# Optimization experiments

Measured on AMD Instinct MI355X. Metric: run time of the kernel, lower is better.

The kernel has to match this reference:

```python
import jax, jax.numpy as jnp
import numpy as np

B, S, NH, D_IN = 64, 512, 4, 256   # batch, seq_len, rnn n_head, input_dim
H = 256                            # hidden_dim == attention activation_dim
AH = 256                           # attention_hidden_dim (attn out_dim)
OUT = 3                            # output_dim (sentiment classes)


def setup_inputs() -> dict:
    key = jax.random.key(0)
    ks = jax.random.split(key, 9)
    def p(k, shape, scale=0.05):
        return jax.random.normal(k, shape, dtype=jnp.float32) * scale
    return dict(
        x=jax.random.normal(ks[0], (B, S, NH, D_IN), dtype=jnp.float32),
        Wk=p(ks[1], (D_IN, H)), bk=jnp.zeros((H,), jnp.float32),
        Wq=p(ks[2], (H, H)),    bq=jnp.zeros((H,), jnp.float32),
        w_mlp=p(ks[3], (2 * H,)),
        Wproj=p(ks[4], (H, AH)), bproj=jnp.zeros((AH,), jnp.float32),
        W1=p(ks[5], (D_IN + AH, H)), b1=jnp.zeros((H,), jnp.float32),
        W2=p(ks[6], (H, H)),    b2=jnp.zeros((H,), jnp.float32),
        Wo=p(ks[7], (NH * H, OUT)), bo=jnp.zeros((OUT,), jnp.float32),
    )


def _cell(x_t, hidden, params):
    Wk, bk, Wq, bq, w_mlp, Wproj, bproj, W1, b1, W2, b2, Wo, bo = params
    kx = x_t @ Wk + bk           # [B, NH, H]  keys from step input
    qx = hidden @ Wq + bq        # [B, NH, H]  queries from hidden state
    w1, w2 = w_mlp[:H], w_mlp[H:]
    # MLP score: s[b,i,j] = tanh(cat(kx[b,j], qx[b,i]) . w) = tanh(kx[b,j].w1 + qx[b,i].w2)
    score = jnp.tanh((qx @ w2)[:, :, None] + (kx @ w1)[:, None, :])  # [B, NH, NH]
    score = jax.nn.softmax(score, axis=-1)
    attn = jnp.einsum('bij,bjh->bih', score, kx) @ Wproj + bproj     # [B, NH, AH]
    concat = jnp.concatenate([x_t, attn], axis=-1)                   # [B, NH, D_IN+AH]
    hidden_new = jax.nn.relu(concat @ W1 + b1) @ W2 + b2             # [B, NH, H]
    logits = hidden_new.reshape(B, NH * H) @ Wo + bo                 # [B, OUT]
    out = jax.nn.log_softmax(logits, axis=-1)
    return out, hidden_new


def reference(x, Wk, bk, Wq, bq, w_mlp, Wproj, bproj, W1, b1, W2, b2, Wo, bo):
    params = (Wk, bk, Wq, bq, w_mlp, Wproj, bproj, W1, b1, W2, b2, Wo, bo)
    h0 = jnp.zeros((B, NH, H), x.dtype)
    xs = jnp.swapaxes(x, 0, 1)  # [S, B, NH, D_IN] for scan over time
    def step(h, x_t):
        out, h_new = _cell(x_t, h, params)
        return h_new, out
    h_final, outs = jax.lax.scan(step, h0, xs)
    # return_sequence=False: last-step log-softmax output and final hidden
    return outs[-1], h_final
```

## Files before the change

### kernel.cpp

```cpp
#include <hip/hip_runtime.h>
#include <hip/hip_bf16.h>
#include <math.h>

#define BB   64
#define SS   512
#define NHH  4
#define DD   256
#define HH   256
#define LDH  264

typedef __attribute__((ext_vector_type(8))) short  short8;
typedef __attribute__((ext_vector_type(4))) float  floatx4;

#define OFF_V2     0
#define OFF_CB1    256
#define OFF_C2     512
#define OFF_CKW    513
#define OFF_QW     768
#define OFF_WK1    1024
#define OFF_BKP    1280
#define OFF_VT     1536
#define OFF_RU     1792
#define OFF_WFUSE  67328
#define OFF_WKF    132864
#define OFF_PACK   198400
#define OFF_CH     263936

__device__ __forceinline__ unsigned short f2b(float f) {
  __hip_bfloat16 h = __float2bfloat16(f);
  return __builtin_bit_cast(unsigned short, h);
}
__device__ __forceinline__ float b2f(unsigned short u) {
  unsigned v = (unsigned)u << 16;
  return __builtin_bit_cast(float, v);
}

__global__ __launch_bounds__(256) void initA_kernel(
    const float* __restrict__ Wproj, const float* __restrict__ W1,
    const float* __restrict__ bk, const float* __restrict__ bproj,
    const float* __restrict__ Wq, const float* __restrict__ w_mlp,
    float* __restrict__ ws)
{
  int tid = threadIdx.x;
  int bx = blockIdx.x;
  const float* W1b = W1 + 256 * 256;
  if (bx < 256) {
    __shared__ float row[256];
    row[tid] = Wproj[bx * 256 + tid];
    __syncthreads();
    float acc = 0.f;
#pragma unroll 8
    for (int k = 0; k < 256; ++k)
      acc = fmaf(row[k], W1b[k * 256 + tid], acc);
    ws[OFF_WFUSE + bx * 256 + tid] = acc;
  } else if (bx == 256) {
    float acc = bproj[tid];
#pragma unroll 8
    for (int k = 0; k < 256; ++k)
      acc = fmaf(bk[k], Wproj[k * 256 + tid], acc);
    ws[OFF_BKP + tid] = acc;
  } else {
    const float4* Wq4 = (const float4*)(Wq + tid * 256);
    const float4* w24 = (const float4*)(w_mlp + 256);
    float a = 0.f;
    for (int k = 0; k < 64; ++k) {
      float4 wv = Wq4[k], xv = w24[k];
      a = fmaf(wv.x, xv.x, fmaf(wv.y, xv.y, fmaf(wv.z, xv.z, fmaf(wv.w, xv.w, a))));
    }
    ws[OFF_VT + tid] = a;
  }
}

__global__ __launch_bounds__(256) void initB_kernel(
    const float* __restrict__ Wk, const float* __restrict__ W1,
    const float* __restrict__ b1, const float* __restrict__ W2,
    const float* __restrict__ b2, const float* __restrict__ bq,
    const float* __restrict__ bk, const float* __restrict__ w_mlp,
    float* __restrict__ ws)
{
  int tid = threadIdx.x;
  int bx = blockIdx.x;
  if (bx < 256) {
    __shared__ float row[256];
    row[tid] = Wk[bx * 256 + tid];
    __syncthreads();
    float acc = 0.f;
    const float* Wf = ws + OFF_WFUSE;
#pragma unroll 8
    for (int k = 0; k < 256; ++k)
      acc = fmaf(row[k], Wf[k * 256 + tid], acc);
    ws[OFF_WKF + bx * 256 + tid] = acc;
  } else if (bx == 256) {
    const float* W1b = W1 + 256 * 256;
    float acc = b1[tid];
#pragma unroll 8
    for (int k = 0; k < 256; ++k)
      acc = fmaf(ws[OFF_BKP + k], W1b[k * 256 + tid], acc);
    ws[OFF_CB1 + tid] = acc;
  } else if (bx == 257) {
    __shared__ float red[256];
    {
      const float4* W24 = (const float4*)(W2 + tid * 256);
      const float4* v4  = (const float4*)(ws + OFF_VT);
      float a = 0.f;
      for (int k = 0; k < 64; ++k) {
        float4 wv = W24[k], xv = v4[k];
        a = fmaf(wv.x, xv.x, fmaf(wv.y, xv.y, fmaf(wv.z, xv.z, fmaf(wv.w, xv.w, a))));
      }
      ws[OFF_V2 + tid] = a;
    }
    red[tid] = bq[tid] * w_mlp[256 + tid];
    __syncthreads();
    for (int s = 128; s; s >>= 1) { if (tid < s) red[tid] += red[tid + s]; __syncthreads(); }
    float s2 = red[0];
    __syncthreads();
    ws[OFF_QW + tid] = s2;
    red[tid] = b2[tid] * ws[OFF_VT + tid];
    __syncthreads();
    for (int s = 128; s; s >>= 1) { if (tid < s) red[tid] += red[tid + s]; __syncthreads(); }
    if (tid == 0) ws[OFF_C2] = red[0] + s2;
    __syncthreads();
    red[tid] = bk[tid] * w_mlp[tid];
    __syncthreads();
    for (int s = 128; s; s >>= 1) { if (tid < s) red[tid] += red[tid + s]; __syncthreads(); }
    if (tid == 0) ws[OFF_CKW] = red[0];
  } else {
    const float4* Wk4 = (const float4*)(Wk + tid * 256);
    const float4* w14 = (const float4*)(w_mlp);
    float a = 0.f;
    for (int k = 0; k < 64; ++k) {
      float4 wv = Wk4[k], xv = w14[k];
      a = fmaf(wv.x, xv.x, fmaf(wv.y, xv.y, fmaf(wv.z, xv.z, fmaf(wv.w, xv.w, a))));
    }
    ws[OFF_WK1 + tid] = a;
  }
}

__global__ __launch_bounds__(256) void initC_kernel(
    const float* __restrict__ W1, float* __restrict__ ws)
{
  int idx = blockIdx.x * 256 + threadIdx.x;
  int mat = idx >> 16;
  int rem = idx & 65535;
  int j    = rem & 7;
  int lane = (rem >> 3) & 63;
  int ks   = (rem >> 9) & 7;
  int pan  = rem >> 12;
  int k = ks * 32 + ((lane >> 4) << 3) + j;
  int n = pan * 16 + (lane & 15);
  float v = (mat == 0) ? ws[OFF_WKF + k * 256 + n] : W1[k * 256 + n];
  ((unsigned short*)(ws + OFF_PACK))[idx] = f2b(v);
}

__device__ __forceinline__ void mfma_gemm4(
    const unsigned short* A_lds, const short8* __restrict__ Bp,
    const float* __restrict__ bias, floatx4 acc[4][4], int l, int w)
{
  int col = l & 15, quad = l >> 4;
#pragma unroll
  for (int pp = 0; pp < 4; ++pp) {
    float bv = bias ? bias[(w * 4 + pp) * 16 + col] : 0.f;
#pragma unroll
    for (int mf = 0; mf < 4; ++mf)
      acc[mf][pp] = (floatx4){bv, bv, bv, bv};
  }
  const short8* Bb = Bp + (size_t)(w * 4) * 512 + l;
  short8 bb[3][4];
#pragma unroll
  for (int pp = 0; pp < 4; ++pp) bb[0][pp] = Bb[pp * 512];
#pragma unroll
  for (int pp = 0; pp < 4; ++pp) bb[1][pp] = Bb[pp * 512 + 64];
#pragma unroll
  for (int kb = 0; kb < 8; ++kb) {
    if (kb + 2 < 8) {
#pragma unroll
      for (int pp = 0; pp < 4; ++pp)
        bb[(kb + 2) % 3][pp] = Bb[pp * 512 + (kb + 2) * 64];
    }
    short8 aa[4];
#pragma unroll
    for (int mf = 0; mf < 4; ++mf)
      aa[mf] = *(const short8*)(A_lds + (mf * 16 + col) * LDH + kb * 32 + quad * 8);
#pragma unroll
    for (int mf = 0; mf < 4; ++mf)
#pragma unroll
      for (int pp = 0; pp < 4; ++pp)
        acc[mf][pp] = __builtin_amdgcn_mfma_f32_16x16x32_bf16(
            aa[mf], bb[kb % 3][pp], acc[mf][pp], 0, 0, 0);
  }
}

__device__ __forceinline__ void acc_to_lds(
    unsigned short* D, const floatx4 acc[4][4], int l, int w)
{
  int col = l & 15, quad = l >> 4;
#pragma unroll
  for (int mf = 0; mf < 4; ++mf)
#pragma unroll
    for (int pp = 0; pp < 4; ++pp)
#pragma unroll
      for (int r = 0; r < 4; ++r)
        D[(mf * 16 + quad * 4 + r) * LDH + (w * 4 + pp) * 16 + col] = f2b(acc[mf][pp][r]);
}

__device__ __forceinline__ void lds_to_global_bf16(
    const unsigned short* S, unsigned short* __restrict__ g, int b, int tt, int tid)
{
#pragma unroll
  for (int it = 0; it < 8; ++it) {
    int u8 = it * 256 + tid;
    int r = u8 >> 5;
    int c8 = u8 & 31;
    int t = tt * 16 + (r >> 2), head = r & 3;
    float4 v = *(const float4*)&S[r * LDH + c8 * 8];
    *(float4*)&g[(((size_t)t * 64 + b) * 4 + head) * 256 + c8 * 8] = v;
  }
}

__global__ __launch_bounds__(256, 2) void pre_kernel(
    const float* __restrict__ x, const float* __restrict__ ws,
    float* __restrict__ kw_c, unsigned short* __restrict__ xw1_c,
    unsigned short* __restrict__ kpw_c, int t0)
{
  __shared__ float kwbuf[256];
  __shared__ __align__(16) unsigned short XS[64 * LDH];

  int b  = blockIdx.x & 63;
  int tt = blockIdx.x >> 6;
  int tid = threadIdx.x;
  int l = tid & 63, w = tid >> 6;

  const float4* xsrc = (const float4*)(x + (size_t)(b * SS + t0 + tt * 16) * NHH * DD);
#pragma unroll
  for (int i = 0; i < 16; ++i) {
    int f4 = i * 256 + tid;
    int r = f4 >> 6, c4 = f4 & 63;
    float4 v = xsrc[f4];
    ushort4 h;
    h.x = f2b(v.x); h.y = f2b(v.y); h.z = f2b(v.z); h.w = f2b(v.w);
    *(ushort4*)&XS[r * LDH + c4 * 4] = h;
  }
  __syncthreads();

  const short8* wp0 = (const short8*)((const unsigned short*)(ws + OFF_PACK));
  const short8* wp1 = (const short8*)((const unsigned short*)(ws + OFF_PACK) + 65536);

  {
    float part = 0.f;
    const unsigned short* trow = XS + l * LDH + w * 64;
#pragma unroll
    for (int j8 = 0; j8 < 8; ++j8) {
      short8 tv = *(const short8*)(trow + j8 * 8);
#pragma unroll
      for (int j = 0; j < 8; ++j)
        part = fmaf(b2f((unsigned short)tv[j]), ws[OFF_WK1 + w * 64 + j8 * 8 + j], part);
    }
    kwbuf[l * 4 + w] = part;
  }

  floatx4 acc1[4][4], acc2[4][4];
  mfma_gemm4(XS, wp0, nullptr, acc1, l, w);
  mfma_gemm4(XS, wp1, ws + OFF_CB1, acc2, l, w);
  __syncthreads();

  if (tid < 64) {
    float s = kwbuf[tid * 4] + kwbuf[tid * 4 + 1] + kwbuf[tid * 4 + 2] + kwbuf[tid * 4 + 3]
            + ws[OFF_CKW];
    kw_c[((size_t)(tt * 16 + (tid >> 2)) * 64 + b) * 4 + (tid & 3)] = s;
  }

  acc_to_lds(XS, acc1, l, w);
  __syncthreads();
  lds_to_global_bf16(XS, kpw_c, b, tt, tid);
  __syncthreads();
  acc_to_lds(XS, acc2, l, w);
  __syncthreads();
  lds_to_global_bf16(XS, xw1_c, b, tt, tid);
}

__device__ __forceinline__ float wave_reduce_sum(float x) {
#define DPPSTEP(ctrl, rmask)                                                   \
  {                                                                            \
    int _s = __builtin_amdgcn_update_dpp(0, __builtin_bit_cast(int, x),        \
                                         (ctrl), (rmask), 0xf, true);          \
    x += __builtin_bit_cast(float, _s);                                        \
  }
  DPPSTEP(0x111, 0xf)
  DPPSTEP(0x112, 0xf)
  DPPSTEP(0x114, 0xf)
  DPPSTEP(0x118, 0xf)
  DPPSTEP(0x142, 0xa)
  DPPSTEP(0x143, 0xc)
#undef DPPSTEP
  return __builtin_bit_cast(float, __builtin_amdgcn_readlane(__builtin_bit_cast(int, x), 63));
}

__device__ __forceinline__ float tanh_fast(float y) {
  float ex = __expf(2.f * y);
  return 1.f - 2.f * __builtin_amdgcn_rcpf(ex + 1.f);
}

__global__ __launch_bounds__(256, 1) void seq_kernel(
    const unsigned short* __restrict__ xw1_c, const unsigned short* __restrict__ kpw_c,
    const float* __restrict__ kw_c, float* __restrict__ ws,
    float* __restrict__ relu_u, int t0, int n)
{
  int b = blockIdx.x & 63;
  int i = blockIdx.x >> 6;
  int tid = threadIdx.x;
  int wv = tid >> 6, l = tid & 63;
  int ngroups = n >> 3;

  if (wv == 0) {
    float4 v2v = ((const float4*)(ws + OFF_V2))[l];
    float c2 = ws[OFF_C2];
    float qw = ws[OFF_QW + b * 4 + i];

    const ushort4* xw = (const ushort4*)xw1_c;
    const ushort4* kp = (const ushort4*)kpw_c;

    struct Slot { ushort4 x, k0, k1, k2, k3; float4 kw; };

    auto load = [&](Slot& s, int tc) {
      size_t rb_ = (size_t)(tc * 64 + b) * 4;
      s.x  = xw[(rb_ + i) * 64 + l];
      s.k0 = kp[(rb_ + 0) * 64 + l];
      s.k1 = kp[(rb_ + 1) * 64 + l];
      s.k2 = kp[(rb_ + 2) * 64 + l];
      s.k3 = kp[(rb_ + 3) * 64 + l];
      s.kw = *(const float4*)&kw_c[rb_];
    };

    auto step = [&](Slot& s, int t) {
      float e0 = tanh_fast(qw + s.kw.x);
      float e1 = tanh_fast(qw + s.kw.y);
      float e2 = tanh_fast(qw + s.kw.z);
      float e3 = tanh_fast(qw + s.kw.w);
      float q0 = __expf(e0), q1 = __expf(e1), q2 = __expf(e2), q3 = __expf(e3);
      float inv = __builtin_amdgcn_rcpf(q0 + q1 + q2 + q3);
      float4 K0 = {b2f(s.k0.x), b2f(s.k0.y), b2f(s.k0.z), b2f(s.k0.w)};
      float4 K1 = {b2f(s.k1.x), b2f(s.k1.y), b2f(s.k1.z), b2f(s.k1.w)};
      float4 K2 = {b2f(s.k2.x), b2f(s.k2.y), b2f(s.k2.z), b2f(s.k2.w)};
      float4 K3 = {b2f(s.k3.x), b2f(s.k3.y), b2f(s.k3.z), b2f(s.k3.w)};
      float4 X  = {b2f(s.x.x), b2f(s.x.y), b2f(s.x.z), b2f(s.x.w)};
      float4 a;
      a.x = fmaf(q0, K0.x, fmaf(q1, K1.x, fmaf(q2, K2.x, q3 * K3.x)));
      a.y = fmaf(q0, K0.y, fmaf(q1, K1.y, fmaf(q2, K2.y, q3 * K3.y)));
      a.z = fmaf(q0, K0.z, fmaf(q1, K1.z, fmaf(q2, K2.z, q3 * K3.z)));
      a.w = fmaf(q0, K0.w, fmaf(q1, K1.w, fmaf(q2, K2.w, q3 * K3.w)));
      float4 u;
      u.x = fmaf(a.x, inv, X.x); u.y = fmaf(a.y, inv, X.y);
      u.z = fmaf(a.z, inv, X.z); u.w = fmaf(a.w, inv, X.w);
      float4 r;
      r.x = fmaxf(u.x, 0.f); r.y = fmaxf(u.y, 0.f);
      r.z = fmaxf(u.z, 0.f); r.w = fmaxf(u.w, 0.f);
      float d = fmaf(r.x, v2v.x, fmaf(r.y, v2v.y, fmaf(r.z, v2v.z, r.w * v2v.w)));
      qw = wave_reduce_sum(d) + c2;
      if (t0 + t == SS - 1)
        *(float4*)&relu_u[(size_t)(b * 4 + i) * 256 + l * 4] = r;
    };

    Slot s[8];
#pragma unroll
    for (int j = 0; j < 8; ++j) load(s[j], j < n ? j : n - 1);

    for (int g = 0; g < ngroups; ++g) {
      int t = g * 8;
#pragma unroll
      for (int j = 0; j < 8; ++j) {
        step(s[j], t + j);
        int nt = t + 8 + j;
        load(s[j], nt < n ? nt : n - 1);
      }
      __builtin_amdgcn_s_barrier();
    }
    if (l == 0) ws[OFF_QW + b * 4 + i] = qw;
  } else {
    float4 f4[9];
    float4 sacc = {0.f, 0.f, 0.f, 0.f};
#pragma unroll
    for (int q = 0; q < 9; ++q) f4[q] = (float4){0.f, 0.f, 0.f, 0.f};

    for (int g = 0; g < ngroups; ++g) {
#pragma unroll
      for (int q = 0; q < 9; ++q) {
        sacc.x += f4[q].x; sacc.y += f4[q].y;
        sacc.z += f4[q].z; sacc.w += f4[q].w;
      }
      int tbase = g * 8 + 16;
#pragma unroll
      for (int tl = 0; tl < 3; ++tl) {
        int tloc = (wv - 1) + 3 * tl; if (tloc > 7) tloc = 7;
        int t = tbase + tloc; if (t > n - 1) t = n - 1;
        size_t rb_ = (size_t)(t * 64 + b) * 4;
        const float4* kpb = (const float4*)(kpw_c + rb_ * 256);
        f4[tl * 3 + 0] = kpb[l];
        f4[tl * 3 + 1] = kpb[64 + l];
        const float4* xwb = (const float4*)(xw1_c + (rb_ + i) * 256);
        const float4* kwb = (const float4*)(kw_c + rb_);
        f4[tl * 3 + 2] = (l < 32) ? xwb[l] : kwb[0];
      }
      __builtin_amdgcn_s_barrier();
    }
    float z = sacc.x + sacc.y + sacc.z + sacc.w;
    asm volatile("" :: "v"(z));
  }
}

__global__ __launch_bounds__(256) void final_hidden_kernel(
    const float* __restrict__ relu_u, const float* __restrict__ W2,
    const float* __restrict__ b2, float* __restrict__ out)
{
  __shared__ float rs[256];
  int row = blockIdx.x;
  int tid = threadIdx.x;
  rs[tid] = relu_u[(size_t)row * 256 + tid];
  __syncthreads();
  float acc = b2[tid];
  for (int k = 0; k < 256; ++k) acc = fmaf(rs[k], W2[k * 256 + tid], acc);
  out[192 + (size_t)row * 256 + tid] = acc;
}

__global__ __launch_bounds__(256) void final_logits_kernel(
    const float* __restrict__ hf, const float* __restrict__ Wo,
    const float* __restrict__ bo, float* __restrict__ outp)
{
  __shared__ float r0[256], r1[256], r2[256];
  int b = blockIdx.x;
  int tid = threadIdx.x;
  float a0 = 0.f, a1 = 0.f, a2 = 0.f;
  for (int k = tid; k < 1024; k += 256) {
    float h = hf[(size_t)b * 1024 + k];
    a0 = fmaf(h, Wo[k * 3 + 0], a0);
    a1 = fmaf(h, Wo[k * 3 + 1], a1);
    a2 = fmaf(h, Wo[k * 3 + 2], a2);
  }
  r0[tid] = a0; r1[tid] = a1; r2[tid] = a2;
  __syncthreads();
  for (int s = 128; s; s >>= 1) {
    if (tid < s) { r0[tid] += r0[tid + s]; r1[tid] += r1[tid + s]; r2[tid] += r2[tid + s]; }
    __syncthreads();
  }
  if (tid == 0) {
    float l0 = r0[0] + bo[0], l1 = r1[0] + bo[1], l2 = r2[0] + bo[2];
    float m = fmaxf(l0, fmaxf(l1, l2));
    float lse = m + logf(expf(l0 - m) + expf(l1 - m) + expf(l2 - m));
    outp[b * 3 + 0] = l0 - lse;
    outp[b * 3 + 1] = l1 - lse;
    outp[b * 3 + 2] = l2 - lse;
  }
}

extern "C" void kernel_launch(void* const* d_in, const int* in_sizes, int n_in,
                              void* d_out, int out_size, void* d_ws, size_t ws_size,
                              hipStream_t stream)
{
  const float* x     = (const float*)d_in[0];
  const float* Wk    = (const float*)d_in[1];
  const float* bk    = (const float*)d_in[2];
  const float* Wq    = (const float*)d_in[3];
  const float* bq    = (const float*)d_in[4];
  const float* w_mlp = (const float*)d_in[5];
  const float* Wproj = (const float*)d_in[6];
  const float* bproj = (const float*)d_in[7];
  const float* W1    = (const float*)d_in[8];
  const float* b1    = (const float*)d_in[9];
  const float* W2    = (const float*)d_in[10];
  const float* b2    = (const float*)d_in[11];
  const float* Wo    = (const float*)d_in[12];
  const float* bo    = (const float*)d_in[13];
  float* out = (float*)d_out;
  float* ws  = (float*)d_ws;

  float* ru = ws + OFF_RU;
  const long per_t = 256 + 65536;

  long ws_floats = (long)(ws_size / 4);
  long avail = ws_floats - (long)OFF_CH;

  int Tc = SS;
  while (Tc > 16 && (long)Tc * per_t > avail) Tc -= 16;

  float* kw_c = ws + OFF_CH;
  unsigned short* xw1_c = (unsigned short*)(kw_c + (size_t)Tc * 256);
  unsigned short* kpw_c = xw1_c + (size_t)Tc * 65536;

  initA_kernel<<<258, 256, 0, stream>>>(Wproj, W1, bk, bproj, Wq, w_mlp, ws);
  initB_kernel<<<259, 256, 0, stream>>>(Wk, W1, b1, W2, b2, bq, bk, w_mlp, ws);
  initC_kernel<<<512, 256, 0, stream>>>(W1, ws);

  for (int t0 = 0; t0 < SS; t0 += Tc) {
    int n = (SS - t0) < Tc ? (SS - t0) : Tc;
    pre_kernel<<<64 * (n / 16), 256, 0, stream>>>(x, ws, kw_c, xw1_c, kpw_c, t0);
    seq_kernel<<<256, 256, 0, stream>>>(xw1_c, kpw_c, kw_c, ws, ru, t0, n);
  }

  final_hidden_kernel<<<BB * NHH, 256, 0, stream>>>(ru, W2, b2, out);
  final_logits_kernel<<<BB, 256, 0, stream>>>(out + 192, Wo, bo, out);
}
```

Before: 466.3 us.

## Stage recurrence inputs through an LDS ring filled by producer waves

The sequential kernel now has three producer waves load per-step key/input projections from global memory, convert bf16 to fp32, and write them into a 24-slot shared-memory ring. The single compute wave reads from LDS with double-buffered registers instead of keeping 8 in-flight global loads. This replaces the earlier prefetch-only warming waves, aiming to hide global latency from the serial dependency chain at the cost of LDS traffic and block-wide barriers every 8 steps. The pre-kernel also reuses one accumulator set with a separate LDS staging buffer so the two GEMMs are written out sequentially, lowering register pressure.

```diff
diff --git a/kernel.cpp b/kernel.cpp
--- a/kernel.cpp
+++ b/kernel.cpp
@@ -224,6 +224,7 @@
 {
   __shared__ float kwbuf[256];
   __shared__ __align__(16) unsigned short XS[64 * LDH];
+  __shared__ __align__(16) unsigned short TS[64 * LDH];
 
   int b  = blockIdx.x & 63;
   int tt = blockIdx.x >> 6;
@@ -232,8 +233,8 @@
 
   const float4* xsrc = (const float4*)(x + (size_t)(b * SS + t0 + tt * 16) * NHH * DD);
 #pragma unroll
-  for (int i = 0; i < 16; ++i) {
-    int f4 = i * 256 + tid;
+  for (int it = 0; it < 16; ++it) {
+    int f4 = it * 256 + tid;
     int r = f4 >> 6, c4 = f4 & 63;
     float4 v = xsrc[f4];
     ushort4 h;
@@ -258,24 +259,23 @@
     kwbuf[l * 4 + w] = part;
   }
 
-  floatx4 acc1[4][4], acc2[4][4];
-  mfma_gemm4(XS, wp0, nullptr, acc1, l, w);
-  mfma_gemm4(XS, wp1, ws + OFF_CB1, acc2, l, w);
+  floatx4 acc[4][4];
+
+  mfma_gemm4(XS, wp0, nullptr, acc, l, w);
+  acc_to_lds(TS, acc, l, w);
   __syncthreads();
-
   if (tid < 64) {
     float s = kwbuf[tid * 4] + kwbuf[tid * 4 + 1] + kwbuf[tid * 4 + 2] + kwbuf[tid * 4 + 3]
             + ws[OFF_CKW];
     kw_c[((size_t)(tt * 16 + (tid >> 2)) * 64 + b) * 4 + (tid & 3)] = s;
   }
-
-  acc_to_lds(XS, acc1, l, w);
+  lds_to_global_bf16(TS, kpw_c, b, tt, tid);
+
+  mfma_gemm4(XS, wp1, ws + OFF_CB1, acc, l, w);
   __syncthreads();
-  lds_to_global_bf16(XS, kpw_c, b, tt, tid);
+  acc_to_lds(TS, acc, l, w);
   __syncthreads();
-  acc_to_lds(XS, acc2, l, w);
-  __syncthreads();
-  lds_to_global_bf16(XS, xw1_c, b, tt, tid);
+  lds_to_global_bf16(TS, xw1_c, b, tt, tid);
 }
 
 __device__ __forceinline__ float wave_reduce_sum(float x) {
@@ -300,49 +300,84 @@
   return 1.f - 2.f * __builtin_amdgcn_rcpf(ex + 1.f);
 }
 
+#define RING  24
+#define SLOT  1284
+
 __global__ __launch_bounds__(256, 1) void seq_kernel(
     const unsigned short* __restrict__ xw1_c, const unsigned short* __restrict__ kpw_c,
     const float* __restrict__ kw_c, float* __restrict__ ws,
     float* __restrict__ relu_u, int t0, int n)
 {
+  __shared__ float ring[RING * SLOT];
   int b = blockIdx.x & 63;
   int i = blockIdx.x >> 6;
   int tid = threadIdx.x;
   int wv = tid >> 6, l = tid & 63;
   int ngroups = n >> 3;
 
-  if (wv == 0) {
+  if (wv != 0) {
+    int tsel = wv - 1;
+    auto fill = [&](int t) {
+      if (t >= n) return;
+      size_t rb = (size_t)(t * 64 + b) * 4;
+      float* slot = ring + (t % RING) * SLOT;
+      ushort4 h0 = ((const ushort4*)(kpw_c + (rb + 0) * 256))[l];
+      ushort4 h1 = ((const ushort4*)(kpw_c + (rb + 1) * 256))[l];
+      ushort4 h2 = ((const ushort4*)(kpw_c + (rb + 2) * 256))[l];
+      ushort4 h3 = ((const ushort4*)(kpw_c + (rb + 3) * 256))[l];
+      ushort4 hx = ((const ushort4*)(xw1_c + (rb + i) * 256))[l];
+      float4 kwv = *(const float4*)(kw_c + rb);
+      *(float4*)&slot[0 * 256 + l * 4] = (float4){b2f(h0.x), b2f(h0.y), b2f(h0.z), b2f(h0.w)};
+      *(float4*)&slot[1 * 256 + l * 4] = (float4){b2f(h1.x), b2f(h1.y), b2f(h1.z), b2f(h1.w)};
+      *(float4*)&slot[2 * 256 + l * 4] = (float4){b2f(h2.x), b2f(h2.y), b2f(h2.z), b2f(h2.w)};
+      *(float4*)&slot[3 * 256 + l * 4] = (float4){b2f(h3.x), b2f(h3.y), b2f(h3.z), b2f(h3.w)};
+      *(float4*)&slot[4 * 256 + l * 4] = (float4){b2f(hx.x), b2f(hx.y), b2f(hx.z), b2f(hx.w)};
+      if (l == 0) *(float4*)&slot[1280] = kwv;
+    };
+    for (int tl = tsel; tl < 16; tl += 3) fill(tl);
+    __syncthreads();
+    for (int g = 0; g < ngroups; ++g) {
+      int base = (g + 2) * 8;
+      fill(base + tsel);
+      fill(base + tsel + 3);
+      if (tsel < 2) fill(base + tsel + 6);
+      __syncthreads();
+    }
+  } else {
     float4 v2v = ((const float4*)(ws + OFF_V2))[l];
     float c2 = ws[OFF_C2];
     float qw = ws[OFF_QW + b * 4 + i];
 
-    const ushort4* xw = (const ushort4*)xw1_c;
-    const ushort4* kp = (const ushort4*)kpw_c;
-
-    struct Slot { ushort4 x, k0, k1, k2, k3; float4 kw; };
-
-    auto load = [&](Slot& s, int tc) {
-      size_t rb_ = (size_t)(tc * 64 + b) * 4;
-      s.x  = xw[(rb_ + i) * 64 + l];
-      s.k0 = kp[(rb_ + 0) * 64 + l];
-      s.k1 = kp[(rb_ + 1) * 64 + l];
-      s.k2 = kp[(rb_ + 2) * 64 + l];
-      s.k3 = kp[(rb_ + 3) * 64 + l];
-      s.kw = *(const float4*)&kw_c[rb_];
+    float4 K0a, K1a, K2a, K3a, Xa, KWa;
+    float4 K0b, K1b, K2b, K3b, Xb, KWb;
+
+    auto rdA = [&](int t) {
+      const float* slot = ring + (t % RING) * SLOT;
+      K0a = *(const float4*)&slot[0 * 256 + l * 4];
+      K1a = *(const float4*)&slot[1 * 256 + l * 4];
+      K2a = *(const float4*)&slot[2 * 256 + l * 4];
+      K3a = *(const float4*)&slot[3 * 256 + l * 4];
+      Xa  = *(const float4*)&slot[4 * 256 + l * 4];
+      KWa = *(const float4*)&slot[1280];
     };
-
-    auto step = [&](Slot& s, int t) {
-      float e0 = tanh_fast(qw + s.kw.x);
-      float e1 = tanh_fast(qw + s.kw.y);
-      float e2 = tanh_fast(qw + s.kw.z);
-      float e3 = tanh_fast(qw + s.kw.w);
+    auto rdB = [&](int t) {
+      const float* slot = ring + (t % RING) * SLOT;
+      K0b = *(const float4*)&slot[0 * 256 + l * 4];
+      K1b = *(const float4*)&slot[1 * 256 + l * 4];
+      K2b = *(const float4*)&slot[2 * 256 + l * 4];
+      K3b = *(const float4*)&slot[3 * 256 + l * 4];
+      Xb  = *(const float4*)&slot[4 * 256 + l * 4];
+      KWb = *(const float4*)&slot[1280];
+    };
+
+    auto step = [&](const float4& K0, const float4& K1, const float4& K2,
+                    const float4& K3, const float4& X, const float4& KW, int t) {
+      float e0 = tanh_fast(qw + KW.x);
+      float e1 = tanh_fast(qw + KW.y);
+      float e2 = tanh_fast(qw + KW.z);
+      float e3 = tanh_fast(qw + KW.w);
       float q0 = __expf(e0), q1 = __expf(e1), q2 = __expf(e2), q3 = __expf(e3);
       float inv = __builtin_amdgcn_rcpf(q0 + q1 + q2 + q3);
-      float4 K0 = {b2f(s.k0.x), b2f(s.k0.y), b2f(s.k0.z), b2f(s.k0.w)};
-      float4 K1 = {b2f(s.k1.x), b2f(s.k1.y), b2f(s.k1.z), b2f(s.k1.w)};
-      float4 K2 = {b2f(s.k2.x), b2f(s.k2.y), b2f(s.k2.z), b2f(s.k2.w)};
-      float4 K3 = {b2f(s.k3.x), b2f(s.k3.y), b2f(s.k3.z), b2f(s.k3.w)};
-      float4 X  = {b2f(s.x.x), b2f(s.x.y), b2f(s.x.z), b2f(s.x.w)};
       float4 a;
       a.x = fmaf(q0, K0.x, fmaf(q1, K1.x, fmaf(q2, K2.x, q3 * K3.x)));
       a.y = fmaf(q0, K0.y, fmaf(q1, K1.y, fmaf(q2, K2.y, q3 * K3.y)));
@@ -360,50 +395,24 @@
         *(float4*)&relu_u[(size_t)(b * 4 + i) * 256 + l * 4] = r;
     };
 
-    Slot s[8];
-#pragma unroll
-    for (int j = 0; j < 8; ++j) load(s[j], j < n ? j : n - 1);
-
+    __syncthreads();
+    rdA(0);
     for (int g = 0; g < ngroups; ++g) {
       int t = g * 8;
-#pragma unroll
-      for (int j = 0; j < 8; ++j) {
-        step(s[j], t + j);
-        int nt = t + 8 + j;
-        load(s[j], nt < n ? nt : n - 1);
-      }
-      __builtin_amdgcn_s_barrier();
+      int c1 = t + 1, c2i = t + 2, c3 = t + 3, c4 = t + 4;
+      int c5 = t + 5, c6 = t + 6, c7 = t + 7;
+      int c8 = (t + 8 < n) ? t + 8 : n - 1;
+      rdB(c1);  step(K0a, K1a, K2a, K3a, Xa, KWa, t);
+      rdA(c2i); step(K0b, K1b, K2b, K3b, Xb, KWb, t + 1);
+      rdB(c3);  step(K0a, K1a, K2a, K3a, Xa, KWa, t + 2);
+      rdA(c4);  step(K0b, K1b, K2b, K3b, Xb, KWb, t + 3);
+      rdB(c5);  step(K0a, K1a, K2a, K3a, Xa, KWa, t + 4);
+      rdA(c6);  step(K0b, K1b, K2b, K3b, Xb, KWb, t + 5);
+      rdB(c7);  step(K0a, K1a, K2a, K3a, Xa, KWa, t + 6);
+      rdA(c8);  step(K0b, K1b, K2b, K3b, Xb, KWb, t + 7);
+      __syncthreads();
     }
     if (l == 0) ws[OFF_QW + b * 4 + i] = qw;
-  } else {
-    float4 f4[9];
-    float4 sacc = {0.f, 0.f, 0.f, 0.f};
-#pragma unroll
-    for (int q = 0; q < 9; ++q) f4[q] = (float4){0.f, 0.f, 0.f, 0.f};
-
-    for (int g = 0; g < ngroups; ++g) {
-#pragma unroll
-      for (int q = 0; q < 9; ++q) {
-        sacc.x += f4[q].x; sacc.y += f4[q].y;
-        sacc.z += f4[q].z; sacc.w += f4[q].w;
-      }
-      int tbase = g * 8 + 16;
-#pragma unroll
-      for (int tl = 0; tl < 3; ++tl) {
-        int tloc = (wv - 1) + 3 * tl; if (tloc > 7) tloc = 7;
-        int t = tbase + tloc; if (t > n - 1) t = n - 1;
-        size_t rb_ = (size_t)(t * 64 + b) * 4;
-        const float4* kpb = (const float4*)(kpw_c + rb_ * 256);
-        f4[tl * 3 + 0] = kpb[l];
-        f4[tl * 3 + 1] = kpb[64 + l];
-        const float4* xwb = (const float4*)(xw1_c + (rb_ + i) * 256);
-        const float4* kwb = (const float4*)(kw_c + rb_);
-        f4[tl * 3 + 2] = (l < 32) ? xwb[l] : kwb[0];
-      }
-      __builtin_amdgcn_s_barrier();
-    }
-    float z = sacc.x + sacc.y + sacc.z + sacc.w;
-    asm volatile("" :: "v"(z));
   }
 }
 
```

Result: faster. 447.8 us (-4.0%).
